# Kernel tuning notes

Hardware: AMD Instinct MI355X
Metric: run time of the kernel (lower is better)

## Reference

```python
import jax, jax.numpy as jnp
import numpy as np


def _conv1x1(x, w, b):
    # x: (B, C, H, W), w: (O, C), b: (O,) -> (B, O, H, W)
    return jnp.einsum('bchw,oc->bohw', x, w) + b[None, :, None, None]


def setup_inputs() -> dict:
    key = jax.random.key(0)
    ks = jax.random.split(key, 9)
    C, Cb = 256, 128
    B, H, W = 4, 64, 64
    s_in = 1.0 / np.sqrt(C)   # kaiming-uniform-ish scale for 1x1 convs
    s_bn = 1.0 / np.sqrt(Cb)
    return {
        'x': jax.random.normal(ks[0], (B, C, H, W), dtype=jnp.float32),
        'theta_w': jax.random.uniform(ks[1], (Cb, C), jnp.float32, -s_in, s_in),
        'theta_b': jax.random.uniform(ks[2], (Cb,), jnp.float32, -s_in, s_in),
        'phi_w': jax.random.uniform(ks[3], (Cb, C), jnp.float32, -s_in, s_in),
        'phi_b': jax.random.uniform(ks[4], (Cb,), jnp.float32, -s_in, s_in),
        'g_w': jax.random.uniform(ks[5], (Cb, C), jnp.float32, -s_in, s_in),
        'g_b': jax.random.uniform(ks[6], (Cb,), jnp.float32, -s_in, s_in),
        'W_w': jax.random.uniform(ks[7], (C, Cb), jnp.float32, -s_bn, s_bn),
        'W_b': jax.random.uniform(ks[8], (C,), jnp.float32, -s_bn, s_bn),
    }


def reference(x, theta_w, theta_b, phi_w, phi_b, g_w, g_b, W_w, W_b):
    B, C, H, Wd = x.shape
    Cb = theta_w.shape[0]
    # NOTE: the original uses raw torch.reshape (row-major), NOT transpose,
    # so (B, Cb, H, W) -> (B, H*W, Cb) scrambles channel/spatial layout.
    # We replicate that exactly with jnp.reshape.
    theta = _conv1x1(x, theta_w, theta_b).reshape(B, -1, Cb)   # (B, N, Cb)
    phi = _conv1x1(x, phi_w, phi_b).reshape(B, Cb, -1)         # (B, Cb, N)
    g = _conv1x1(x, g_w, g_b).reshape(B, -1, Cb)               # (B, N, Cb)
    scores = jnp.einsum('bnc,bcm->bnm', theta, phi)            # (B, N, N)
    attn = jax.nn.softmax(scores, axis=1)                      # softmax over dim=1 (unusual axis)
    y = jnp.einsum('bnm,bmc->bnc', attn, g)                    # (B, N, Cb)
    y = y.reshape(B, -1, H, Wd)                                # raw reshape back to (B, Cb, H, W)
    w = _conv1x1(y, W_w, W_b)                                  # (B, C, H, W)
    return w + x
```

## Files before the change

kernel.cpp:

```cpp
#include <hip/hip_runtime.h>
#include <math.h>

constexpr int CI = 256;
constexpr int CB = 128;
constexpr int HWD = 4096;
constexpr int NBATCH = 4;
constexpr int NN_ = 4096;
constexpr size_t U1 = (size_t)NBATCH * NN_ * CB;
constexpr size_t U_THETA = 0;
constexpr size_t U_PHIT  = U1;
constexpr size_t U_G     = 2 * U1;
constexpr size_t U_GT    = 3 * U1;
constexpr size_t U_Y     = 4 * U1;
constexpr size_t U_XT    = 4 * U1;
constexpr size_t U_WCAT  = 8 * U1;
constexpr size_t U_WW    = 8 * U1 + 98304;
constexpr size_t F_D     = (8 * U1 + 131072) / 2;

typedef short v8s __attribute__((ext_vector_type(8)));
typedef unsigned short u8s __attribute__((ext_vector_type(8)));
typedef unsigned int v4u __attribute__((ext_vector_type(4)));
typedef float v4f __attribute__((ext_vector_type(4)));
typedef float v16f __attribute__((ext_vector_type(16)));
#define MFMA16(a, b, c) __builtin_amdgcn_mfma_f32_16x16x32_bf16(a, b, c, 0, 0, 0)
#define MFMA32(a, b, c) __builtin_amdgcn_mfma_f32_32x32x16_bf16(a, b, c, 0, 0, 0)

__device__ __forceinline__ unsigned short f2bf(float f) {
    union { float f; unsigned u; } v; v.f = f;
    unsigned r = v.u + 0x7fff + ((v.u >> 16) & 1);
    return (unsigned short)(r >> 16);
}
__device__ __forceinline__ float bf2f(unsigned short s) {
    union { unsigned u; float f; } v; v.u = (unsigned)s << 16;
    return v.f;
}
__device__ __forceinline__ unsigned pack2bf(float lo, float hi) {
    return (unsigned)f2bf(lo) | ((unsigned)f2bf(hi) << 16);
}
__device__ __forceinline__ void pl32swap(unsigned &a, unsigned &b) {
    asm volatile("v_permlane32_swap_b32 %0, %1" : "+v"(a), "+v"(b));
}
__device__ __forceinline__ v8s pack_swap(float p0, float p1, float p2, float p3,
                                         float p4, float p5, float p6, float p7) {
    unsigned c0 = pack2bf(p0, p1), c1 = pack2bf(p2, p3);
    unsigned c2 = pack2bf(p4, p5), c3 = pack2bf(p6, p7);
    pl32swap(c0, c2);
    pl32swap(c1, c3);
    union { v4u u; v8s s; } r;
    r.u[0] = c0; r.u[1] = c1; r.u[2] = c2; r.u[3] = c3;
    return r.s;
}

__global__ __launch_bounds__(256) void k0_xpose(
    const float* __restrict__ x, unsigned short* __restrict__ xT,
    const float* __restrict__ tw, const float* __restrict__ pw,
    const float* __restrict__ gw, const float* __restrict__ Ww,
    unsigned short* __restrict__ wcat, unsigned short* __restrict__ wwB)
{
    __shared__ unsigned short T[64 * 72];
    const int t = threadIdx.x;
    if (blockIdx.y == 4) {
        int wb = blockIdx.x + 64 * blockIdx.z;
        if (t < 128) {
            int e = (wb * 128 + t) * 4;
            const float* src; unsigned short* dst;
            if (e < 32768)       { src = tw + e;           dst = wcat + e; }
            else if (e < 65536)  { src = pw + (e - 32768); dst = wcat + e; }
            else if (e < 98304)  { src = gw + (e - 65536); dst = wcat + e; }
            else                 { src = Ww + (e - 98304); dst = wwB + (e - 98304); }
            float4 f = *(const float4*)src;
            ushort4 u;
            u.x = f2bf(f.x); u.y = f2bf(f.y); u.z = f2bf(f.z); u.w = f2bf(f.w);
            *(ushort4*)dst = u;
        }
        return;
    }
    const int hw0 = blockIdx.x * 64, c0 = blockIdx.y * 64, b = blockIdx.z;
    const float* xb = x + (size_t)b * CI * HWD;
    const int rr = t >> 4, cc = t & 15;
    #pragma unroll
    for (int pass = 0; pass < 4; pass++) {
        float4 f = *(const float4*)&xb[(size_t)(c0 + pass * 16 + rr) * HWD + hw0 + cc * 4];
        T[(cc * 4 + 0) * 72 + pass * 16 + rr] = f2bf(f.x);
        T[(cc * 4 + 1) * 72 + pass * 16 + rr] = f2bf(f.y);
        T[(cc * 4 + 2) * 72 + pass * 16 + rr] = f2bf(f.z);
        T[(cc * 4 + 3) * 72 + pass * 16 + rr] = f2bf(f.w);
    }
    __syncthreads();
    const int row = t >> 2, cs = (t & 3) * 16;
    unsigned short* dst = xT + (size_t)b * NN_ * CI;
    #pragma unroll
    for (int h = 0; h < 2; h++)
        *(u8s*)&dst[(size_t)(hw0 + row) * CI + c0 + cs + h * 8] =
            *(const u8s*)&T[row * 72 + cs + h * 8];
}

__global__ __launch_bounds__(256, 4) void k1_mfma(
    const unsigned short* __restrict__ xT, const unsigned short* __restrict__ wcat,
    const float* __restrict__ tb, const float* __restrict__ pb,
    const float* __restrict__ gb,
    unsigned short* __restrict__ thetaB, unsigned short* __restrict__ phiTB,
    unsigned short* __restrict__ gB)
{
    __shared__ unsigned short LdsX[64 * 268];
    unsigned short* T = LdsX;
    const int t = threadIdx.x;
    const int lane = t & 63, w = t >> 6;
    const int l31 = lane & 31, lh = lane >> 5;
    const int qj = w >> 1, qh = w & 1;
    const int hw0 = blockIdx.x * 64, j0 = blockIdx.y * 64, b = blockIdx.z;
    const int matId = j0 >> 7, jl0 = j0 & 127;
    const float* bvec = (matId == 0) ? tb : (matId == 1) ? pb : gb;
    const unsigned short* xb = xT + (size_t)b * NN_ * CI;

    {
        const int row = t >> 2, seg = t & 3;
        #pragma unroll
        for (int c8 = 0; c8 < 8; c8++)
            *(u8s*)&LdsX[row * 268 + seg * 64 + c8 * 8] =
                *(const u8s*)&xb[(size_t)(hw0 + row) * CI + seg * 64 + c8 * 8];
    }
    __syncthreads();

    v16f s = {};
    #pragma unroll
    for (int kt = 0; kt < 16; kt++) {
        v8s a = *(const v8s*)&wcat[(size_t)(j0 + qj * 32 + l31) * CI + kt * 16 + lh * 8];
        v8s bx = *(const v8s*)&LdsX[(qh * 32 + l31) * 268 + kt * 16 + lh * 8];
        s = MFMA32(a, bx, s);
    }

    if (matId != 1) {
        unsigned short* dst = ((matId == 0) ? thetaB : gB) + (size_t)b * CB * HWD;
        #pragma unroll
        for (int reg = 0; reg < 16; reg++) {
            int row = (reg & 3) + 8 * (reg >> 2) + 4 * lh;
            int cb = jl0 + qj * 32 + row;
            dst[(size_t)cb * HWD + hw0 + qh * 32 + l31] = f2bf(s[reg] + bvec[cb]);
        }
    } else {
        __syncthreads();
        #pragma unroll
        for (int reg = 0; reg < 16; reg++) {
            int row = (reg & 3) + 8 * (reg >> 2) + 4 * lh;
            T[(qh * 32 + l31) * 76 + qj * 32 + row] =
                f2bf(s[reg] + bvec[jl0 + qj * 32 + row]);
        }
        __syncthreads();
        unsigned short* dst = phiTB + (size_t)b * NN_ * CB;
        const int row = t >> 2, cs = (t & 3) * 16;
        #pragma unroll
        for (int h = 0; h < 2; h++)
            *(u8s*)&dst[(size_t)(hw0 + row) * CB + jl0 + cs + h * 8] =
                *(const u8s*)&T[row * 76 + cs + h * 8];
    }
}

__global__ __launch_bounds__(256, 2) void k2_colsum(
    const unsigned short* __restrict__ thetaB,
    const unsigned short* __restrict__ phiTB,
    float* __restrict__ Dout)
{
    __shared__ float part[4][128];
    const int t = threadIdx.x;
    const int lane = t & 63, w = t >> 6;
    const int ln = lane & 15, quad = lane >> 4;
    const int m0 = blockIdx.x * 128, q = blockIdx.y, b = blockIdx.z;
    const unsigned short* th = thetaB + (size_t)b * NN_ * CB;
    const unsigned short* ph = phiTB + (size_t)b * NN_ * CB;

    v8s bf[8][4];
    #pragma unroll
    for (int mt = 0; mt < 8; mt++)
        #pragma unroll
        for (int kt = 0; kt < 4; kt++)
            bf[mt][kt] = *(const v8s*)&ph[(size_t)(m0 + mt * 16 + ln) * CB + kt * 32 + quad * 8];

    float dsum[8] = {};
    const int nBeg = q * 1024 + w * 16, nEnd = q * 1024 + 1024;
    v8s af[4], afn[4];
    #pragma unroll
    for (int kt = 0; kt < 4; kt++)
        af[kt] = *(const v8s*)&th[(size_t)(nBeg + ln) * CB + kt * 32 + quad * 8];
    for (int n0 = nBeg; n0 < nEnd; n0 += 64) {
        int nn = (n0 + 64 < nEnd) ? n0 + 64 : nBeg;
        #pragma unroll
        for (int kt = 0; kt < 4; kt++)
            afn[kt] = *(const v8s*)&th[(size_t)(nn + ln) * CB + kt * 32 + quad * 8];
        #pragma unroll
        for (int mt = 0; mt < 8; mt++) {
            v4f s = {};
            #pragma unroll
            for (int kt = 0; kt < 4; kt++)
                s = MFMA16(af[kt], bf[mt][kt], s);
            #pragma unroll
            for (int r = 0; r < 4; r++)
                dsum[mt] += __expf(s[r]);
        }
        #pragma unroll
        for (int kt = 0; kt < 4; kt++) af[kt] = afn[kt];
    }
    #pragma unroll
    for (int mt = 0; mt < 8; mt++) {
        float v = dsum[mt];
        v += __shfl_xor(v, 16);
        v += __shfl_xor(v, 32);
        dsum[mt] = v;
    }
    if (quad == 0) {
        #pragma unroll
        for (int mt = 0; mt < 8; mt++) part[w][mt * 16 + ln] = dsum[mt];
    }
    __syncthreads();
    if (t < 128) {
        float v = part[0][t] + part[1][t] + part[2][t] + part[3][t];
        Dout[((size_t)q * NBATCH + b) * NN_ + m0 + t] = v;
    }
}

__global__ __launch_bounds__(256) void k1b_transpose_scale_g(
    const unsigned short* __restrict__ gB, const float* __restrict__ D,
    unsigned short* __restrict__ gTB)
{
    __shared__ unsigned short T[128 * 36];
    const int t = threadIdx.x;
    const int m0 = blockIdx.x * 32;
    const int b  = blockIdx.z;
    const unsigned short* F = gB + (size_t)b * CB * HWD;
    unsigned short* dst = gTB + (size_t)b * CB * HWD;
    const int mrow = t >> 3, cg = t & 7;
    {
        int m = m0 + mrow;
        float d = D[((size_t)0 * NBATCH + b) * NN_ + m]
                + D[((size_t)1 * NBATCH + b) * NN_ + m]
                + D[((size_t)2 * NBATCH + b) * NN_ + m]
                + D[((size_t)3 * NBATCH + b) * NN_ + m];
        float r = 1.0f / d;
        #pragma unroll
        for (int j8 = 0; j8 < 2; j8++) {
            int cbase = cg * 8 + j8 * 64;
            u8s u = *(const u8s*)&F[(size_t)m * CB + cbase];
            #pragma unroll
            for (int e = 0; e < 8; e++)
                T[(cbase + e) * 36 + mrow] = f2bf(bf2f(u[e]) * r);
        }
    }
    __syncthreads();
    const int c = t >> 1, mh = (t & 1) * 16;
    #pragma unroll
    for (int h8 = 0; h8 < 2; h8++)
        *(u8s*)&dst[(size_t)c * HWD + m0 + mh + h8 * 8] =
            *(const u8s*)&T[c * 36 + mh + h8 * 8];
}

__global__ __launch_bounds__(256, 2) void k3_attn(
    const unsigned short* __restrict__ thetaB,
    const unsigned short* __restrict__ phiTB,
    const unsigned short* __restrict__ gTB,
    unsigned short* __restrict__ Y)
{
    __shared__ unsigned short Lphi[2][64 * 134];
    const int t = threadIdx.x;
    const int lane = t & 63, w = t >> 6;
    const int l31 = lane & 31, lh = lane >> 5;
    const int rowS = t >> 4, colS = t & 15;
    const int n0 = blockIdx.x * 128, q = blockIdx.y, b = blockIdx.z;
    const unsigned short* th = thetaB + (size_t)b * NN_ * CB;
    const unsigned short* ph = phiTB + (size_t)b * NN_ * CB;
    const unsigned short* gT = gTB + (size_t)b * CB * HWD;

    v8s ath[8];
    #pragma unroll
    for (int kt = 0; kt < 8; kt++)
        ath[kt] = *(const v8s*)&th[(size_t)(n0 + w * 32 + l31) * CB + kt * 16 + lh * 8];

    const int mBeg = q * 1024;
    v8s preg[4];
    #pragma unroll
    for (int p = 0; p < 4; p++)
        preg[p] = *(const v8s*)&ph[(size_t)(mBeg + p * 16 + rowS) * CB + colS * 8];
    #pragma unroll
    for (int p = 0; p < 4; p++)
        *(v8s*)&Lphi[0][(p * 16 + rowS) * 134 + colS * 8] = preg[p];
    #pragma unroll
    for (int p = 0; p < 4; p++)
        preg[p] = *(const v8s*)&ph[(size_t)(mBeg + 64 + p * 16 + rowS) * CB + colS * 8];
    __syncthreads();

    v16f yacc[4] = {};
    #pragma unroll 2
    for (int it = 0; it < 16; ++it) {
        const int cur = it & 1;
        const int m0 = mBeg + it * 64;
        v8s gfA[2][4];
        #pragma unroll
        for (int ks = 0; ks < 2; ks++)
            #pragma unroll
            for (int ct = 0; ct < 4; ct++)
                gfA[ks][ct] = *(const v8s*)&gT[(size_t)(ct * 32 + l31) * HWD + m0 + ks * 16 + lh * 8];
        v16f st0 = {}, st1 = {};
        #pragma unroll
        for (int kt = 0; kt < 8; kt++) {
            v8s a0 = *(const v8s*)&Lphi[cur][(l31) * 134 + kt * 16 + lh * 8];
            v8s a1 = *(const v8s*)&Lphi[cur][(32 + l31) * 134 + kt * 16 + lh * 8];
            st0 = MFMA32(a0, ath[kt], st0);
            st1 = MFMA32(a1, ath[kt], st1);
        }
        #pragma unroll
        for (int p = 0; p < 4; p++)
            *(v8s*)&Lphi[cur ^ 1][(p * 16 + rowS) * 134 + colS * 8] = preg[p];
        __syncthreads();
        {
            const int mP = mBeg + ((it + 2) & 15) * 64;
            #pragma unroll
            for (int p = 0; p < 4; p++)
                preg[p] = *(const v8s*)&ph[(size_t)(mP + p * 16 + rowS) * CB + colS * 8];
        }
        v8s gfB[2][4];
        #pragma unroll
        for (int ks = 0; ks < 2; ks++)
            #pragma unroll
            for (int ct = 0; ct < 4; ct++)
                gfB[ks][ct] = *(const v8s*)&gT[(size_t)(ct * 32 + l31) * HWD + m0 + 32 + ks * 16 + lh * 8];
        v8s apv0 = pack_swap(__expf(st0[0]),  __expf(st0[1]),  __expf(st0[2]),  __expf(st0[3]),
                             __expf(st0[4]),  __expf(st0[5]),  __expf(st0[6]),  __expf(st0[7]));
        v8s apv1 = pack_swap(__expf(st0[8]),  __expf(st0[9]),  __expf(st0[10]), __expf(st0[11]),
                             __expf(st0[12]), __expf(st0[13]), __expf(st0[14]), __expf(st0[15]));
        v8s apv2 = pack_swap(__expf(st1[0]),  __expf(st1[1]),  __expf(st1[2]),  __expf(st1[3]),
                             __expf(st1[4]),  __expf(st1[5]),  __expf(st1[6]),  __expf(st1[7]));
        v8s apv3 = pack_swap(__expf(st1[8]),  __expf(st1[9]),  __expf(st1[10]), __expf(st1[11]),
                             __expf(st1[12]), __expf(st1[13]), __expf(st1[14]), __expf(st1[15]));
        #pragma unroll
        for (int ct = 0; ct < 4; ct++) yacc[ct] = MFMA32(apv0, gfA[0][ct], yacc[ct]);
        #pragma unroll
        for (int ct = 0; ct < 4; ct++) yacc[ct] = MFMA32(apv1, gfA[1][ct], yacc[ct]);
        #pragma unroll
        for (int ct = 0; ct < 4; ct++) yacc[ct] = MFMA32(apv2, gfB[0][ct], yacc[ct]);
        #pragma unroll
        for (int ct = 0; ct < 4; ct++) yacc[ct] = MFMA32(apv3, gfB[1][ct], yacc[ct]);
    }
    unsigned short* yp = Y + ((size_t)q * NBATCH + b) * CB * HWD;
    #pragma unroll
    for (int ct = 0; ct < 4; ct++)
        #pragma unroll
        for (int reg = 0; reg < 16; reg++) {
            int row = (reg & 3) + 8 * (reg >> 2) + 4 * lh;
            yp[(size_t)(n0 + w * 32 + row) * CB + ct * 32 + l31] = f2bf(yacc[ct][reg]);
        }
}

__global__ __launch_bounds__(256, 2) void k4_mfma(
    const float* __restrict__ x, const unsigned short* __restrict__ wwB,
    const float* __restrict__ Wb, const unsigned short* __restrict__ Ybuf,
    float* __restrict__ out)
{
    __shared__ unsigned short Yt[64 * 136];
    const int t = threadIdx.x;
    const int lane = t & 63, w = t >> 6;
    const int ln = lane & 15, quad = lane >> 4;
    const int hw0 = blockIdx.x * 64, o0 = blockIdx.y * 128, b = blockIdx.z;

    const int cb = t >> 1, seg = (t & 1) * 32;
    #pragma unroll
    for (int g8 = 0; g8 < 4; g8++) {
        float sum[8] = {};
        #pragma unroll
        for (int q = 0; q < 4; q++) {
            u8s u = *(const u8s*)&Ybuf[((size_t)q * NBATCH + b) * CB * HWD +
                                       (size_t)cb * HWD + hw0 + seg + g8 * 8];
            #pragma unroll
            for (int j = 0; j < 8; j++) sum[j] += bf2f(u[j]);
        }
        #pragma unroll
        for (int j = 0; j < 8; j++)
            Yt[(seg + g8 * 8 + j) * 136 + cb] = f2bf(sum[j]);
    }
    __syncthreads();

    v8s aw[2][4];
    #pragma unroll
    for (int os = 0; os < 2; os++)
        #pragma unroll
        for (int kt = 0; kt < 4; kt++)
            aw[os][kt] = *(const v8s*)&wwB[(size_t)(o0 + w * 32 + os * 16 + ln) * CB + kt * 32 + quad * 8];

    v4f s[2][4] = {};
    #pragma unroll
    for (int kt = 0; kt < 4; kt++) {
        v8s by[4];
        #pragma unroll
        for (int mt = 0; mt < 4; mt++)
            by[mt] = *(const v8s*)&Yt[(mt * 16 + ln) * 136 + kt * 32 + quad * 8];
        #pragma unroll
        for (int os = 0; os < 2; os++)
            #pragma unroll
            for (int mt = 0; mt < 4; mt++)
                s[os][mt] = MFMA16(aw[os][kt], by[mt], s[os][mt]);
    }
    #pragma unroll
    for (int os = 0; os < 2; os++)
        #pragma unroll
        for (int mt = 0; mt < 4; mt++)
            #pragma unroll
            for (int r = 0; r < 4; r++) {
                int o = o0 + w * 32 + os * 16 + quad * 4 + r;
                size_t idx = (size_t)b * CI * HWD + (size_t)o * HWD + hw0 + mt * 16 + ln;
                out[idx] = s[os][mt][r] + Wb[o] + x[idx];
            }
}

extern "C" void kernel_launch(void* const* d_in, const int* in_sizes, int n_in,
                              void* d_out, int out_size, void* d_ws, size_t ws_size,
                              hipStream_t stream)
{
    const float* x  = (const float*)d_in[0];
    const float* tw = (const float*)d_in[1];
    const float* tb = (const float*)d_in[2];
    const float* pw = (const float*)d_in[3];
    const float* pb = (const float*)d_in[4];
    const float* gw = (const float*)d_in[5];
    const float* gb = (const float*)d_in[6];
    const float* Ww = (const float*)d_in[7];
    const float* Wb = (const float*)d_in[8];
    unsigned short* wsu = (unsigned short*)d_ws;
    float* wsf = (float*)d_ws;
    unsigned short* thetaB = wsu + U_THETA;
    unsigned short* phiTB  = wsu + U_PHIT;
    unsigned short* gB     = wsu + U_G;
    unsigned short* gTB    = wsu + U_GT;
    unsigned short* Ybuf   = wsu + U_Y;
    unsigned short* xTB    = wsu + U_XT;
    unsigned short* wcatB  = wsu + U_WCAT;
    unsigned short* wwB    = wsu + U_WW;
    float* Dbuf = wsf + F_D;
    float* out = (float*)d_out;
    dim3 blk(256, 1, 1);
    hipLaunchKernelGGL(k0_xpose, dim3(64, 5, NBATCH), blk, 0, stream,
                       x, xTB, tw, pw, gw, Ww, wcatB, wwB);
    hipLaunchKernelGGL(k1_mfma, dim3(64, 6, NBATCH), blk, 0, stream,
                       xTB, wcatB, tb, pb, gb, thetaB, phiTB, gB);
    hipLaunchKernelGGL(k2_colsum, dim3(32, 4, NBATCH), blk, 0, stream,
                       thetaB, phiTB, Dbuf);
    hipLaunchKernelGGL(k1b_transpose_scale_g, dim3(128, 1, NBATCH), blk, 0, stream,
                       gB, Dbuf, gTB);
    hipLaunchKernelGGL(k3_attn, dim3(32, 4, NBATCH), blk, 0, stream,
                       thetaB, phiTB, gTB, Ybuf);
    hipLaunchKernelGGL(k4_mfma, dim3(64, 2, NBATCH), blk, 0, stream,
                       x, wwB, Wb, Ybuf, out);
}
```

Baseline: 211.4 us.

## Split attention key range across two warp groups with in-block LDS reduction

The attention kernel now launches 512 threads per block, and two groups of four waves each process half of the block's 1024-key range with separate double-buffered phi tiles in LDS. The partial Y accumulators of group 1 are written to shared memory, and group 0 adds them in before writing bf16 output. This raises the number of waves per block and halves the serial loop length, aiming to hide latency better. In exchange it uses twice the LDS per block, adds a reduction step, and the launch bounds of (512,4) may force register spilling given the large accumulator and fragment arrays.

```diff
diff --git a/kernel.cpp b/kernel.cpp
--- a/kernel.cpp
+++ b/kernel.cpp
@@ -253,17 +253,20 @@
             *(const u8s*)&T[c * 36 + mh + h8 * 8];
 }
 
-__global__ __launch_bounds__(256, 2) void k3_attn(
+__global__ __launch_bounds__(512, 4) void k3_attn(
     const unsigned short* __restrict__ thetaB,
     const unsigned short* __restrict__ phiTB,
     const unsigned short* __restrict__ gTB,
     unsigned short* __restrict__ Y)
 {
-    __shared__ unsigned short Lphi[2][64 * 134];
-    const int t = threadIdx.x;
-    const int lane = t & 63, w = t >> 6;
+    __shared__ unsigned short Lphi[2][2][64 * 134];
+    const int t = threadIdx.x;
+    const int lane = t & 63;
+    const int w = (t >> 6) & 3;
+    const int g = t >> 8;
     const int l31 = lane & 31, lh = lane >> 5;
-    const int rowS = t >> 4, colS = t & 15;
+    const int tl = t & 255;
+    const int rowS = tl >> 4, colS = tl & 15;
     const int n0 = blockIdx.x * 128, q = blockIdx.y, b = blockIdx.z;
     const unsigned short* th = thetaB + (size_t)b * NN_ * CB;
     const unsigned short* ph = phiTB + (size_t)b * NN_ * CB;
@@ -274,14 +277,14 @@
     for (int kt = 0; kt < 8; kt++)
         ath[kt] = *(const v8s*)&th[(size_t)(n0 + w * 32 + l31) * CB + kt * 16 + lh * 8];
 
-    const int mBeg = q * 1024;
+    const int mBeg = q * 1024 + g * 512;
     v8s preg[4];
     #pragma unroll
     for (int p = 0; p < 4; p++)
         preg[p] = *(const v8s*)&ph[(size_t)(mBeg + p * 16 + rowS) * CB + colS * 8];
     #pragma unroll
     for (int p = 0; p < 4; p++)
-        *(v8s*)&Lphi[0][(p * 16 + rowS) * 134 + colS * 8] = preg[p];
+        *(v8s*)&Lphi[g][0][(p * 16 + rowS) * 134 + colS * 8] = preg[p];
     #pragma unroll
     for (int p = 0; p < 4; p++)
         preg[p] = *(const v8s*)&ph[(size_t)(mBeg + 64 + p * 16 + rowS) * CB + colS * 8];
@@ -289,7 +292,7 @@
 
     v16f yacc[4] = {};
     #pragma unroll 2
-    for (int it = 0; it < 16; ++it) {
+    for (int it = 0; it < 8; ++it) {
         const int cur = it & 1;
         const int m0 = mBeg + it * 64;
         v8s gfA[2][4];
@@ -301,17 +304,17 @@
         v16f st0 = {}, st1 = {};
         #pragma unroll
         for (int kt = 0; kt < 8; kt++) {
-            v8s a0 = *(const v8s*)&Lphi[cur][(l31) * 134 + kt * 16 + lh * 8];
-            v8s a1 = *(const v8s*)&Lphi[cur][(32 + l31) * 134 + kt * 16 + lh * 8];
+            v8s a0 = *(const v8s*)&Lphi[g][cur][(l31) * 134 + kt * 16 + lh * 8];
+            v8s a1 = *(const v8s*)&Lphi[g][cur][(32 + l31) * 134 + kt * 16 + lh * 8];
             st0 = MFMA32(a0, ath[kt], st0);
             st1 = MFMA32(a1, ath[kt], st1);
         }
         #pragma unroll
         for (int p = 0; p < 4; p++)
-            *(v8s*)&Lphi[cur ^ 1][(p * 16 + rowS) * 134 + colS * 8] = preg[p];
+            *(v8s*)&Lphi[g][cur ^ 1][(p * 16 + rowS) * 134 + colS * 8] = preg[p];
         __syncthreads();
         {
-            const int mP = mBeg + ((it + 2) & 15) * 64;
+            const int mP = mBeg + ((it + 2) & 7) * 64;
             #pragma unroll
             for (int p = 0; p < 4; p++)
                 preg[p] = *(const v8s*)&ph[(size_t)(mP + p * 16 + rowS) * CB + colS * 8];
@@ -339,14 +342,26 @@
         #pragma unroll
         for (int ct = 0; ct < 4; ct++) yacc[ct] = MFMA32(apv3, gfB[1][ct], yacc[ct]);
     }
-    unsigned short* yp = Y + ((size_t)q * NBATCH + b) * CB * HWD;
-    #pragma unroll
-    for (int ct = 0; ct < 4; ct++)
-        #pragma unroll
-        for (int reg = 0; reg < 16; reg++) {
-            int row = (reg & 3) + 8 * (reg >> 2) + 4 * lh;
-            yp[(size_t)(n0 + w * 32 + row) * CB + ct * 32 + l31] = f2bf(yacc[ct][reg]);
-        }
+    float* red = (float*)&Lphi[0][0][0];
+    if (g == 1) {
+        #pragma unroll
+        for (int ct = 0; ct < 4; ct++)
+            #pragma unroll
+            for (int reg = 0; reg < 16; reg++)
+                red[w * 4096 + (ct * 16 + reg) * 64 + lane] = yacc[ct][reg];
+    }
+    __syncthreads();
+    if (g == 0) {
+        unsigned short* yp = Y + ((size_t)q * NBATCH + b) * CB * HWD;
+        #pragma unroll
+        for (int ct = 0; ct < 4; ct++)
+            #pragma unroll
+            for (int reg = 0; reg < 16; reg++) {
+                float v = yacc[ct][reg] + red[w * 4096 + (ct * 16 + reg) * 64 + lane];
+                int row = (reg & 3) + 8 * (reg >> 2) + 4 * lh;
+                yp[(size_t)(n0 + w * 32 + row) * CB + ct * 32 + l31] = f2bf(v);
+            }
+    }
 }
 
 __global__ __launch_bounds__(256, 2) void k4_mfma(
@@ -435,6 +450,7 @@
     float* Dbuf = wsf + F_D;
     float* out = (float*)d_out;
     dim3 blk(256, 1, 1);
+    dim3 blk512(512, 1, 1);
     hipLaunchKernelGGL(k0_xpose, dim3(64, 5, NBATCH), blk, 0, stream,
                        x, xTB, tw, pw, gw, Ww, wcatB, wwB);
     hipLaunchKernelGGL(k1_mfma, dim3(64, 6, NBATCH), blk, 0, stream,
@@ -443,7 +459,7 @@
                        thetaB, phiTB, Dbuf);
     hipLaunchKernelGGL(k1b_transpose_scale_g, dim3(128, 1, NBATCH), blk, 0, stream,
                        gB, Dbuf, gTB);
-    hipLaunchKernelGGL(k3_attn, dim3(32, 4, NBATCH), blk, 0, stream,
+    hipLaunchKernelGGL(k3_attn, dim3(32, 4, NBATCH), blk512, 0, stream,
                        thetaB, phiTB, gTB, Ybuf);
     hipLaunchKernelGGL(k4_mfma, dim3(64, 2, NBATCH), blk, 0, stream,
                        x, wwB, Wb, Ybuf, out);
```

Result: slower. 498.5 us (+135.8%).
